# Kernel tuning notes

Measured on AMD Instinct MI355X. Metric: run time of the kernel, lower is better.

## Reference

```python
import jax, jax.numpy as jnp
import numpy as np

B, C, H, W = 32, 256, 64, 64
MH = 8
E = 524288
TEMPERATURE = 0.1
LN_EPS = 1e-5


def setup_inputs() -> dict:
    key = jax.random.key(0)
    ks = jax.random.split(key, 6)
    n_nodes = B * H * W
    scale = 1.0 / np.sqrt(C).astype(np.float32)
    img = jax.random.normal(ks[0], (B, C, H, W), jnp.float32)
    all_edge = jax.random.randint(ks[1], (2, E), 0, n_nodes, dtype=jnp.int64)
    Wp = jax.random.normal(ks[2], (C, C), jnp.float32) * scale
    bp = jnp.zeros((C,), jnp.float32)
    Wg = jax.random.normal(ks[3], (C, C), jnp.float32) * scale
    bg = jnp.zeros((C,), jnp.float32)
    ln_gamma = jnp.ones((C,), jnp.float32)
    ln_beta = jnp.zeros((C,), jnp.float32)
    diff_query = jax.random.normal(ks[4], (1, 1, C), jnp.float32) * scale  # xavier-ish
    return {"img": img, "all_edge": all_edge, "Wp": Wp, "bp": bp,
            "Wg": Wg, "bg": bg, "ln_gamma": ln_gamma, "ln_beta": ln_beta,
            "diff_query": diff_query, "mask_head": MH}


def _gcn_conv(x, row, col, Wg, bg, num_nodes):
    # PyG GCNConv with add_self_loops=True, symmetric normalization.
    loop = jnp.arange(num_nodes, dtype=row.dtype)
    row = jnp.concatenate([row, loop])
    col = jnp.concatenate([col, loop])
    deg = jnp.zeros((num_nodes,), x.dtype).at[col].add(1.0)
    dinv = jnp.where(deg > 0, jax.lax.rsqrt(deg), 0.0)
    norm = dinv[row] * dinv[col]                      # [E+N]
    xl = x @ Wg                                       # [N, C]
    msg = xl[row] * norm[:, None]                     # gather + scale
    agg = jax.ops.segment_sum(msg, col, num_segments=num_nodes)
    return agg + bg


def reference(img, all_edge, Wp, bp, Wg, bg, ln_gamma, ln_beta, diff_query, mask_head):
    b, c, h, w = img.shape
    node_num = h * w
    num_nodes = b * node_num
    hd = c // mask_head
    # [B,C,H,W] -> [B, N, C]
    x = jnp.transpose(img, (0, 2, 3, 1)).reshape(b, node_num, c)
    x = x @ Wp + bp
    x = x.reshape(num_nodes, c)
    g = _gcn_conv(x, all_edge[0], all_edge[1], Wg, bg, num_nodes)
    g = jax.nn.gelu(g, approximate=False)             # nn.GELU (exact)
    g = g + x
    mu = jnp.mean(g, axis=-1, keepdims=True)
    var = jnp.mean(jnp.square(g - mu), axis=-1, keepdims=True)
    img_graph = (g - mu) * jax.lax.rsqrt(var + LN_EPS) * ln_gamma + ln_beta
    # multi-head adjacency: query [B*MH, 1, hd], keys [B*MH, N, hd]
    q = jnp.broadcast_to(diff_query, (b, 1, c)).reshape(b * mask_head, 1, hd)
    k = img_graph.reshape(b, node_num, mask_head, hd)
    k = jnp.transpose(k, (0, 2, 1, 3)).reshape(b * mask_head, node_num, hd)
    adj = jnp.einsum('bod,bnd->bon', q, k) / TEMPERATURE
    adj = jax.nn.softmax(adj, axis=-1)
    return img_graph, adj
```

## Files before the change

kernel.cpp:

```cpp
#include <hip/hip_runtime.h>
#include <hip/hip_bf16.h>

typedef unsigned short u16;
typedef __attribute__((ext_vector_type(8))) short short8;
typedef __attribute__((ext_vector_type(16))) float f32x16;

#define AS1C(p) ((const __attribute__((address_space(1))) void*)(p))
#define AS3(p)  ((__attribute__((address_space(3))) void*)(p))

constexpr int CC    = 256;
constexpr int HWSZ  = 4096;
constexpr int NNODE = 131072;
constexpr int EEDG  = 524288;
constexpr int CAP   = 32;

__device__ __forceinline__ float bf2f(u16 h){ unsigned u = ((unsigned)h)<<16; float f; __builtin_memcpy(&f,&u,4); return f; }
__device__ __forceinline__ u16 f2bf(float f){ unsigned u; __builtin_memcpy(&u,&f,4); return (u16)((u + 0x7FFFu + ((u>>16)&1u))>>16); }

__device__ __forceinline__ unsigned pkbf(float a, float b){
  float2 t; t.x = a; t.y = b;
  __hip_bfloat162 h = __float22bfloat162_rn(t);
  unsigned u; __builtin_memcpy(&u,&h,4); return u;
}

__device__ __forceinline__ float gelu_fast(float v){
  float y = 0.7978845608f*(v + 0.044715f*v*v*v);
  float e = __expf(2.0f*y);
  float r = __builtin_amdgcn_rcpf(e + 1.0f);
  return 0.5f*v*(2.0f - 2.0f*r);
}

__device__ __forceinline__ void unpack8(uint4 q, float f[8]){
  unsigned w0=q.x,w1=q.y,w2=q.z,w3=q.w;
  unsigned l0=w0<<16, h0=w0&0xffff0000u, l1=w1<<16, h1=w1&0xffff0000u;
  unsigned l2=w2<<16, h2=w2&0xffff0000u, l3=w3<<16, h3=w3&0xffff0000u;
  __builtin_memcpy(&f[0],&l0,4); __builtin_memcpy(&f[1],&h0,4);
  __builtin_memcpy(&f[2],&l1,4); __builtin_memcpy(&f[3],&h1,4);
  __builtin_memcpy(&f[4],&l2,4); __builtin_memcpy(&f[5],&h2,4);
  __builtin_memcpy(&f[6],&l3,4); __builtin_memcpy(&f[7],&h3,4);
}

__global__ __launch_bounds__(256) void transpose_split(const float* __restrict__ src,
                                                       u16* __restrict__ dhi, u16* __restrict__ dlo,
                                                       int R, int Ccols, size_t sb_in, size_t sb_out)
{
  __shared__ float t[64][65];
  const float* s = src + blockIdx.z*sb_in + (size_t)(blockIdx.y*64)*Ccols + blockIdx.x*64;
  size_t obase   = blockIdx.z*sb_out + (size_t)(blockIdx.x*64)*R + blockIdx.y*64;
  int tid = threadIdx.x;
  for (int i=0;i<4;++i){
    int idx = i*256 + tid;
    int r = idx>>4, q = idx&15;
    float4 v = *(const float4*)(s + (size_t)r*Ccols + q*4);
    t[r][q*4+0]=v.x; t[r][q*4+1]=v.y; t[r][q*4+2]=v.z; t[r][q*4+3]=v.w;
  }
  __syncthreads();
  for (int i=0;i<2;++i){
    int idx = i*256 + tid;
    int rr = idx>>3, ch = idx&7;
    u16 hi[8], lo[8];
    for (int j=0;j<8;++j){
      float f = t[ch*8+j][rr];
      u16 h = f2bf(f); hi[j] = h;
      lo[j] = f2bf(f - bf2f(h));
    }
    *(uint4*)(dhi + obase + (size_t)rr*R + ch*8) = *(uint4*)hi;
    if (dlo) *(uint4*)(dlo + obase + (size_t)rr*R + ch*8) = *(uint4*)lo;
  }
}

__global__ __launch_bounds__(256,3) void gemm_t1(const float* __restrict__ img,
                                                 const u16* __restrict__ Bt,
                                                 const float* __restrict__ bias,
                                                 u16* __restrict__ C)
{
  __shared__ u16 As[2][64*32];
  __shared__ u16 Bs[2][256*32];
  const int tid = threadIdx.x, wid = tid>>6, lane = tid&63;
  const int row0 = blockIdx.x*64;
  const int bb = row0>>12, hw0 = row0&4095;
  const float* abase = img + (size_t)bb*CC*HWSZ + hw0;
  const int l31 = lane&31, lh = lane>>5;
  const int mpr = l31;
  const int cb  = wid*8 + lh*4;
  const int cs  = wid ^ (mpr&3);
  const int wa0 = (2*mpr  )*32 + cs*8 + lh*4;
  const int wa1 = (2*mpr+1)*32 + cs*8 + lh*4;

  f32x16 acc[2][2];
  #pragma unroll
  for (int i=0;i<2;++i)
    #pragma unroll
    for (int j=0;j<2;++j)
      #pragma unroll
      for (int e=0;e<16;++e) acc[i][j][e]=0.f;

  float2 arX[4], arY[4];

#define LOADA(dst, kt)                                                                 \
  { _Pragma("unroll")                                                                  \
    for (int i=0;i<4;++i)                                                              \
      dst[i] = *(const float2*)(abase + (size_t)((kt)+cb+i)*HWSZ + 2*mpr); }

#define WRITEA(buf, src)                                                               \
  { uint2 p0, p1;                                                                      \
    p0.x = pkbf(src[0].x, src[1].x); p0.y = pkbf(src[2].x, src[3].x);                  \
    p1.x = pkbf(src[0].y, src[1].y); p1.y = pkbf(src[2].y, src[3].y);                  \
    *(uint2*)&As[buf][wa0] = p0;                                                       \
    *(uint2*)&As[buf][wa1] = p1; }

#define STAGE_B(buf, kt)                                                               \
  { _Pragma("unroll")                                                                  \
    for (int it=0; it<4; ++it){                                                        \
      int qb = (it*4+wid)*64;                                                          \
      int q  = qb + lane;                                                              \
      int m  = q>>2, sc = q&3;                                                         \
      int gs = sc ^ ((m>>1)&3);                                                        \
      __builtin_amdgcn_global_load_lds(AS1C(Bt + (size_t)m*256 + (kt) + gs*8),         \
                                       AS3(&Bs[buf][qb*8]), 16, 0, 0); } }

#define STEP(t, XR, YR)                                                                \
  { const int cur = (t)&1;                                                             \
    if ((t) < 7) STAGE_B(cur^1, ((t)+1)*32)                                            \
    if ((t) < 6) LOADA(YR, ((t)+2)*32)                                                 \
    short8 af[2][2], bfr[2][2];                                                        \
    _Pragma("unroll")                                                                  \
    for (int fm=0; fm<2; ++fm)                                                         \
      _Pragma("unroll")                                                                \
      for (int kh=0; kh<2; ++kh) {                                                     \
        int row = fm*32 + l31;                                                         \
        int sa  = (kh*2 + lh) ^ ((row>>1)&3);                                          \
        af[fm][kh] = *(const short8*)&As[cur][row*32 + sa*8];                          \
      }                                                                                \
    _Pragma("unroll")                                                                  \
    for (int fn=0; fn<2; ++fn)                                                         \
      _Pragma("unroll")                                                                \
      for (int kh=0; kh<2; ++kh) {                                                     \
        int col = wid*64 + fn*32 + l31;                                                \
        int sb  = (kh*2 + lh) ^ ((col>>1)&3);                                          \
        bfr[fn][kh] = *(const short8*)&Bs[cur][col*32 + sb*8];                         \
      }                                                                                \
    _Pragma("unroll")                                                                  \
    for (int kh=0; kh<2; ++kh)                                                         \
      _Pragma("unroll")                                                                \
      for (int fm=0; fm<2; ++fm)                                                       \
        _Pragma("unroll")                                                              \
        for (int fn=0; fn<2; ++fn)                                                     \
          acc[fm][fn] = __builtin_amdgcn_mfma_f32_32x32x16_bf16(af[fm][kh], bfr[fn][kh], acc[fm][fn], 0, 0, 0); \
    if ((t) < 7) {                                                                     \
      WRITEA(cur^1, XR)                                                                \
      if ((t) < 6) { asm volatile("s_waitcnt vmcnt(8) lgkmcnt(0)" ::: "memory"); }     \
      else         { asm volatile("s_waitcnt vmcnt(0) lgkmcnt(0)" ::: "memory"); }     \
      __builtin_amdgcn_s_barrier();                                                    \
      __builtin_amdgcn_sched_barrier(0);                                               \
    } }

  LOADA(arX, 0)
  STAGE_B(0, 0)
  asm volatile("s_waitcnt vmcnt(4)" ::: "memory");
  WRITEA(0, arX)
  LOADA(arX, 32)
  asm volatile("s_waitcnt vmcnt(8) lgkmcnt(0)" ::: "memory");
  __builtin_amdgcn_s_barrier();
  __builtin_amdgcn_sched_barrier(0);

  for (int tt=0; tt<8; tt+=2) {
    STEP(tt,   arX, arY)
    STEP(tt+1, arY, arX)
  }
#undef STEP
#undef STAGE_B
#undef WRITEA
#undef LOADA

  #pragma unroll
  for (int fn=0; fn<2; ++fn) {
    int col = wid*64 + fn*32 + l31;
    float bv = bias ? bias[col] : 0.f;
    #pragma unroll
    for (int fm=0; fm<2; ++fm) {
      int rbase = row0 + fm*32 + 4*lh;
      #pragma unroll
      for (int reg=0; reg<16; ++reg) {
        int row = rbase + (reg&3) + 8*(reg>>2);
        C[(size_t)row*256 + col] = f2bf(acc[fm][fn][reg] + bv);
      }
    }
  }
}

__global__ __launch_bounds__(256,3) void gemm1p(const u16* __restrict__ A,
                                                const u16* __restrict__ Bt,
                                                const float* __restrict__ bias,
                                                u16* __restrict__ C)
{
  __shared__ u16 As[2][64*32];
  __shared__ u16 Bs[2][256*32];
  const int tid = threadIdx.x, wid = tid>>6, lane = tid&63;
  const int row0 = blockIdx.x*64;
  const int l31 = lane&31, lh = lane>>5;

  f32x16 acc[2][2];
  #pragma unroll
  for (int i=0;i<2;++i)
    #pragma unroll
    for (int j=0;j<2;++j)
      #pragma unroll
      for (int e=0;e<16;++e) acc[i][j][e]=0.f;

#define STAGE_AB(buf, kt)                                                              \
  {                                                                                    \
    {                                                                                  \
      int qb = wid*64;                                                                 \
      int q  = qb + lane;                                                              \
      int m  = q>>2, sc = q&3;                                                         \
      int gs = sc ^ ((m>>1)&3);                                                        \
      __builtin_amdgcn_global_load_lds(AS1C(A + (size_t)(row0+m)*256 + (kt) + gs*8),   \
                                       AS3(&As[buf][qb*8]), 16, 0, 0);                 \
    }                                                                                  \
    _Pragma("unroll")                                                                  \
    for (int it=0; it<4; ++it){                                                        \
      int qb = (it*4+wid)*64;                                                          \
      int q  = qb + lane;                                                              \
      int m  = q>>2, sc = q&3;                                                         \
      int gs = sc ^ ((m>>1)&3);                                                        \
      __builtin_amdgcn_global_load_lds(AS1C(Bt + (size_t)m*256 + (kt) + gs*8),         \
                                       AS3(&Bs[buf][qb*8]), 16, 0, 0);                 \
    }                                                                                  \
  }

  STAGE_AB(0, 0)
  asm volatile("s_waitcnt vmcnt(0)" ::: "memory");
  __syncthreads();

  for (int t=0; t<8; ++t) {
    int cur = t&1;
    if (t<7) STAGE_AB(cur^1, (t+1)*32)

    short8 af[2][2], bfr[2][2];
    #pragma unroll
    for (int fm=0; fm<2; ++fm)
      #pragma unroll
      for (int kh=0; kh<2; ++kh) {
        int row = fm*32 + l31;
        int sa  = (kh*2 + lh) ^ ((row>>1)&3);
        af[fm][kh] = *(const short8*)&As[cur][row*32 + sa*8];
      }
    #pragma unroll
    for (int fn=0; fn<2; ++fn)
      #pragma unroll
      for (int kh=0; kh<2; ++kh) {
        int col = wid*64 + fn*32 + l31;
        int sb  = (kh*2 + lh) ^ ((col>>1)&3);
        bfr[fn][kh] = *(const short8*)&Bs[cur][col*32 + sb*8];
      }
    #pragma unroll
    for (int kh=0; kh<2; ++kh)
      #pragma unroll
      for (int fm=0; fm<2; ++fm)
        #pragma unroll
        for (int fn=0; fn<2; ++fn)
          acc[fm][fn] = __builtin_amdgcn_mfma_f32_32x32x16_bf16(af[fm][kh], bfr[fn][kh], acc[fm][fn], 0, 0, 0);
    asm volatile("s_waitcnt vmcnt(0)" ::: "memory");
    __syncthreads();
  }
#undef STAGE_AB

  #pragma unroll
  for (int fn=0; fn<2; ++fn) {
    int col = wid*64 + fn*32 + l31;
    float bv = bias ? bias[col] : 0.f;
    #pragma unroll
    for (int fm=0; fm<2; ++fm) {
      int rbase = row0 + fm*32 + 4*lh;
      #pragma unroll
      for (int reg=0; reg<16; ++reg) {
        int row = rbase + (reg&3) + 8*(reg>>2);
        C[(size_t)row*256 + col] = f2bf(acc[fm][fn][reg] + bv);
      }
    }
  }
}

__global__ void fill_all(const int* __restrict__ row, const int* __restrict__ col,
                         int* __restrict__ cur, int* __restrict__ bucket){
  int e = blockIdx.x*256 + threadIdx.x;
  if (e >= EEDG) return;
  int c = col[e];
  int s = atomicAdd(&cur[c], 1);
  if (s < CAP) bucket[(size_t)c*CAP + s] = row[e];
}
__global__ void calc_dinv(const int* __restrict__ cnt, float* __restrict__ dinv){
  int n = blockIdx.x*256 + threadIdx.x;
  if (n < NNODE) dinv[n] = rsqrtf((float)cnt[n] + 1.0f);
}

__global__ __launch_bounds__(256) void fused_agg(
    const u16* __restrict__ xl, const u16* __restrict__ xhi,
    const int* __restrict__ cnt, const float* __restrict__ dinv, const int* __restrict__ bucket,
    const float* __restrict__ bgv, const float* __restrict__ gam, const float* __restrict__ bet,
    const float* __restrict__ qv, float* __restrict__ outg, float* __restrict__ logits)
{
  const int wid = threadIdx.x>>6, lane = threadIdx.x&63;
  const int half = lane>>5, sl = lane&31;
  const int n = blockIdx.x*8 + wid*2 + half;
  const int c0 = sl*8;
  const float dn = dinv[n];
  int lim = cnt[n]; if (lim > CAP) lim = CAP;

  int rl = bucket[(size_t)n*CAP + sl];
  if (sl >= lim) rl = n;
  float wl = (sl < lim) ? dinv[rl]*dn : 0.0f;

  uint4 qh = *(const uint4*)(xhi + (size_t)n*256 + c0);

  float a[8];
  {
    uint4 q = *(const uint4*)(xl + (size_t)n*256 + c0);
    unpack8(q, a);
    float wself = dn*dn;
    #pragma unroll
    for (int j=0;j<8;++j) a[j] *= wself;
  }

  int limR = (lim + 3) & ~3;
  for (int s=0; s<limR; s+=4) {
    int b0 = half*32 + s;
    int  r0 = __shfl(rl, b0),   r1 = __shfl(rl, b0+1);
    int  r2 = __shfl(rl, b0+2), r3 = __shfl(rl, b0+3);
    float w0 = __shfl(wl, b0),   w1 = __shfl(wl, b0+1);
    float w2 = __shfl(wl, b0+2), w3 = __shfl(wl, b0+3);
    uint4 q0 = *(const uint4*)(xl + (size_t)r0*256 + c0);
    uint4 q1 = *(const uint4*)(xl + (size_t)r1*256 + c0);
    uint4 q2 = *(const uint4*)(xl + (size_t)r2*256 + c0);
    uint4 q3 = *(const uint4*)(xl + (size_t)r3*256 + c0);
    float f0[8], f1[8], f2[8], f3[8];
    unpack8(q0, f0); unpack8(q1, f1); unpack8(q2, f2); unpack8(q3, f3);
    #pragma unroll
    for (int j=0;j<8;++j) a[j] += f0[j]*w0 + f1[j]*w1 + f2[j]*w2 + f3[j]*w3;
  }

  float xv[8];
  unpack8(qh, xv);

  float4 b0v = *(const float4*)(bgv + c0), b1v = *(const float4*)(bgv + c0 + 4);
  float bgs[8] = {b0v.x,b0v.y,b0v.z,b0v.w,b1v.x,b1v.y,b1v.z,b1v.w};
  float g[8];
  float s1 = 0.f, s2 = 0.f;
  #pragma unroll
  for (int j=0;j<8;++j){
    g[j] = gelu_fast(a[j] + bgs[j]) + xv[j];
    s1 += g[j]; s2 += g[j]*g[j];
  }
  #pragma unroll
  for (int off=16; off; off>>=1){ s1 += __shfl_xor(s1, off); s2 += __shfl_xor(s2, off); }
  float mu  = s1*(1.0f/256.0f);
  float var = s2*(1.0f/256.0f) - mu*mu;
  float inv = rsqrtf(var + 1e-5f);

  float4 g0 = *(const float4*)(gam + c0), g1 = *(const float4*)(gam + c0 + 4);
  float4 e0 = *(const float4*)(bet + c0), e1 = *(const float4*)(bet + c0 + 4);
  float gms[8] = {g0.x,g0.y,g0.z,g0.w,g1.x,g1.y,g1.z,g1.w};
  float bts[8] = {e0.x,e0.y,e0.z,e0.w,e1.x,e1.y,e1.z,e1.w};
  float y[8];
  #pragma unroll
  for (int j=0;j<8;++j) y[j] = (g[j]-mu)*inv*gms[j] + bts[j];

  float4 o0 = {y[0],y[1],y[2],y[3]}, o1 = {y[4],y[5],y[6],y[7]};
  *reinterpret_cast<float4*>(outg + (size_t)n*256 + c0)     = o0;
  *reinterpret_cast<float4*>(outg + (size_t)n*256 + c0 + 4) = o1;

  float4 q0 = *(const float4*)(qv + c0), q1 = *(const float4*)(qv + c0 + 4);
  float qs[8] = {q0.x,q0.y,q0.z,q0.w,q1.x,q1.y,q1.z,q1.w};
  float dq = 0.f;
  #pragma unroll
  for (int j=0;j<8;++j) dq += y[j]*qs[j];
  dq += __shfl_xor(dq,1); dq += __shfl_xor(dq,2);
  if ((sl&3)==0){
    int b = n>>12, p = n&4095, h = sl>>2;
    logits[(size_t)(b*8+h)*4096 + p] = dq*10.0f;
  }
}

__global__ __launch_bounds__(256) void softmax_rows(const float* __restrict__ logits, float* __restrict__ outa){
  int r = blockIdx.x;
  const float* p = logits + (size_t)r*4096;
  int tid = threadIdx.x;
  int wid = tid>>6, lane = tid&63;
  __shared__ float redm[4];
  __shared__ float reds[4];
  float v[16];
  float mx = -1e30f;
  for (int i=0;i<16;++i){ v[i] = p[tid + i*256]; mx = fmaxf(mx, v[i]); }
  for (int off=32; off; off>>=1) mx = fmaxf(mx, __shfl_xor(mx, off));
  if (lane==0) redm[wid]=mx;
  __syncthreads();
  mx = fmaxf(fmaxf(redm[0],redm[1]), fmaxf(redm[2],redm[3]));
  float sum = 0.f;
  for (int i=0;i<16;++i){ v[i] = expf(v[i]-mx); sum += v[i]; }
  for (int off=32; off; off>>=1) sum += __shfl_xor(sum, off);
  if (lane==0) reds[wid]=sum;
  __syncthreads();
  sum = reds[0]+reds[1]+reds[2]+reds[3];
  float rinv = 1.0f/sum;
  for (int i=0;i<16;++i) outa[(size_t)r*4096 + tid + i*256] = v[i]*rinv;
}

extern "C" void kernel_launch(void* const* d_in, const int* in_sizes, int n_in,
                              void* d_out, int out_size, void* d_ws, size_t ws_size,
                              hipStream_t stream)
{
  const float* img  = (const float*)d_in[0];
  const int* edges  = (const int*)d_in[1];
  const float* Wp   = (const float*)d_in[2];
  const float* bp   = (const float*)d_in[3];
  const float* Wg   = (const float*)d_in[4];
  const float* bg   = (const float*)d_in[5];
  const float* lng  = (const float*)d_in[6];
  const float* lnb  = (const float*)d_in[7];
  const float* dq   = (const float*)d_in[8];
  char* ws = (char*)d_ws;

  constexpr size_t REG  = (size_t)NNODE*CC*2;
  constexpr size_t WTS  = 2u*131072;
  constexpr size_t GBLK = 524288u*2 + (size_t)NNODE*CAP*4 + (size_t)256*4096*4;
  if (ws_size < 2*REG + WTS + GBLK) return;

  u16* buf0 = (u16*)(ws + 0);
  u16* buf1 = (u16*)(ws + REG);
  char* wts  = ws + 2*REG;
  char* gblk = wts + WTS;

  u16* WpT_hi = (u16*)(wts);
  u16* WgT_hi = (u16*)(wts + 131072);
  int*   cur    = (int*)(gblk);
  float* dinv   = (float*)(gblk + 524288);
  int*   bucket = (int*)(gblk + 1048576);
  float* logits = (float*)(gblk + 1048576 + (size_t)NNODE*CAP*4);

  transpose_split<<<dim3(4,4,1), 256, 0, stream>>>(Wp, WpT_hi, nullptr, 256, 256, 0, 0);
  transpose_split<<<dim3(4,4,1), 256, 0, stream>>>(Wg, WgT_hi, nullptr, 256, 256, 0, 0);

  hipMemsetAsync(cur, 0, 524288, stream);
  fill_all <<<2048, 256, 0, stream>>>(edges, edges+EEDG, cur, bucket);
  calc_dinv<<<512,  256, 0, stream>>>(cur, dinv);

  gemm_t1<<<2048, 256, 0, stream>>>(img, WpT_hi, bp, buf0);
  gemm1p<<<2048, 256, 0, stream>>>(buf0, WgT_hi, nullptr, buf1);

  float* outg = (float*)d_out;
  float* outa = (float*)d_out + (size_t)NNODE*CC;
  fused_agg<<<NNODE/8, 256, 0, stream>>>(buf1, buf0, cur, dinv, bucket,
                                         bg, lng, lnb, dq, outg, logits);
  softmax_rows<<<256, 256, 0, stream>>>(logits, outa);
}
```

Baseline: 230.1 us.

## Fold Wp·Wg into combined weight and compute x and xl in one dual GEMM

Precomputes W2 = Wp·Wg and the folded bias bp·Wg, then uses a single GEMM kernel that reads img once and produces both x (via Wp) and xl (via W2) with two accumulator sets. This removes the second pass over the 64 MB bf16 intermediate x and one kernel launch. In exchange each block uses twice the B-tile LDS and accumulators, and occupancy drops from 3 to 2 blocks per SM. Numerics also change slightly because xl no longer comes from bf16-rounded x.

```diff
diff --git a/kernel.cpp b/kernel.cpp
--- a/kernel.cpp
+++ b/kernel.cpp
@@ -69,13 +69,35 @@
   }
 }
 
-__global__ __launch_bounds__(256,3) void gemm_t1(const float* __restrict__ img,
-                                                 const u16* __restrict__ Bt,
-                                                 const float* __restrict__ bias,
-                                                 u16* __restrict__ C)
+__global__ __launch_bounds__(256) void split_rm(const float* __restrict__ src, u16* __restrict__ dhi)
+{
+  int i = blockIdx.x*256 + threadIdx.x;
+  float4 v = ((const float4*)src)[i];
+  ushort4 h;
+  h.x = f2bf(v.x); h.y = f2bf(v.y); h.z = f2bf(v.z); h.w = f2bf(v.w);
+  ((ushort4*)dhi)[i] = h;
+}
+
+__global__ void bias2_k(const float* __restrict__ bp, const float* __restrict__ Wg,
+                        float* __restrict__ b2)
+{
+  int n = threadIdx.x;
+  float s = 0.f;
+  for (int k=0;k<256;++k) s += bp[k]*Wg[(size_t)k*256 + n];
+  b2[n] = s;
+}
+
+__global__ __launch_bounds__(256,2) void gemm_dual(const float* __restrict__ img,
+                                                   const u16* __restrict__ Btp,
+                                                   const u16* __restrict__ Bt2,
+                                                   const float* __restrict__ bias1,
+                                                   const float* __restrict__ bias2,
+                                                   u16* __restrict__ Cx,
+                                                   u16* __restrict__ Cxl)
 {
   __shared__ u16 As[2][64*32];
-  __shared__ u16 Bs[2][256*32];
+  __shared__ u16 Bsp[2][256*32];
+  __shared__ u16 Bs2[2][256*32];
   const int tid = threadIdx.x, wid = tid>>6, lane = tid&63;
   const int row0 = blockIdx.x*64;
   const int bb = row0>>12, hw0 = row0&4095;
@@ -87,13 +109,13 @@
   const int wa0 = (2*mpr  )*32 + cs*8 + lh*4;
   const int wa1 = (2*mpr+1)*32 + cs*8 + lh*4;
 
-  f32x16 acc[2][2];
+  f32x16 accx[2][2], accl[2][2];
   #pragma unroll
   for (int i=0;i<2;++i)
     #pragma unroll
     for (int j=0;j<2;++j)
       #pragma unroll
-      for (int e=0;e<16;++e) acc[i][j][e]=0.f;
+      for (int e=0;e<16;++e){ accx[i][j][e]=0.f; accl[i][j][e]=0.f; }
 
   float2 arX[4], arY[4];
 
@@ -116,14 +138,16 @@
       int q  = qb + lane;                                                              \
       int m  = q>>2, sc = q&3;                                                         \
       int gs = sc ^ ((m>>1)&3);                                                        \
-      __builtin_amdgcn_global_load_lds(AS1C(Bt + (size_t)m*256 + (kt) + gs*8),         \
-                                       AS3(&Bs[buf][qb*8]), 16, 0, 0); } }
+      __builtin_amdgcn_global_load_lds(AS1C(Btp + (size_t)m*256 + (kt) + gs*8),        \
+                                       AS3(&Bsp[buf][qb*8]), 16, 0, 0);                \
+      __builtin_amdgcn_global_load_lds(AS1C(Bt2 + (size_t)m*256 + (kt) + gs*8),        \
+                                       AS3(&Bs2[buf][qb*8]), 16, 0, 0); } }
 
 #define STEP(t, XR, YR)                                                                \
   { const int cur = (t)&1;                                                             \
     if ((t) < 7) STAGE_B(cur^1, ((t)+1)*32)                                            \
     if ((t) < 6) LOADA(YR, ((t)+2)*32)                                                 \
-    short8 af[2][2], bfr[2][2];                                                        \
+    short8 af[2][2], bp8[2][2], b28[2][2];                                             \
     _Pragma("unroll")                                                                  \
     for (int fm=0; fm<2; ++fm)                                                         \
       _Pragma("unroll")                                                                \
@@ -138,18 +162,21 @@
       for (int kh=0; kh<2; ++kh) {                                                     \
         int col = wid*64 + fn*32 + l31;                                                \
         int sb  = (kh*2 + lh) ^ ((col>>1)&3);                                          \
-        bfr[fn][kh] = *(const short8*)&Bs[cur][col*32 + sb*8];                         \
+        bp8[fn][kh] = *(const short8*)&Bsp[cur][col*32 + sb*8];                        \
+        b28[fn][kh] = *(const short8*)&Bs2[cur][col*32 + sb*8];                        \
       }                                                                                \
     _Pragma("unroll")                                                                  \
     for (int kh=0; kh<2; ++kh)                                                         \
       _Pragma("unroll")                                                                \
       for (int fm=0; fm<2; ++fm)                                                       \
         _Pragma("unroll")                                                              \
-        for (int fn=0; fn<2; ++fn)                                                     \
-          acc[fm][fn] = __builtin_amdgcn_mfma_f32_32x32x16_bf16(af[fm][kh], bfr[fn][kh], acc[fm][fn], 0, 0, 0); \
+        for (int fn=0; fn<2; ++fn) {                                                   \
+          accx[fm][fn] = __builtin_amdgcn_mfma_f32_32x32x16_bf16(af[fm][kh], bp8[fn][kh], accx[fm][fn], 0, 0, 0); \
+          accl[fm][fn] = __builtin_amdgcn_mfma_f32_32x32x16_bf16(af[fm][kh], b28[fn][kh], accl[fm][fn], 0, 0, 0); \
+        }                                                                              \
     if ((t) < 7) {                                                                     \
       WRITEA(cur^1, XR)                                                                \
-      if ((t) < 6) { asm volatile("s_waitcnt vmcnt(8) lgkmcnt(0)" ::: "memory"); }     \
+      if ((t) < 6) { asm volatile("s_waitcnt vmcnt(4) lgkmcnt(0)" ::: "memory"); }     \
       else         { asm volatile("s_waitcnt vmcnt(0) lgkmcnt(0)" ::: "memory"); }     \
       __builtin_amdgcn_s_barrier();                                                    \
       __builtin_amdgcn_sched_barrier(0);                                               \
@@ -157,10 +184,10 @@
 
   LOADA(arX, 0)
   STAGE_B(0, 0)
-  asm volatile("s_waitcnt vmcnt(4)" ::: "memory");
+  asm volatile("s_waitcnt vmcnt(8)" ::: "memory");
   WRITEA(0, arX)
   LOADA(arX, 32)
-  asm volatile("s_waitcnt vmcnt(8) lgkmcnt(0)" ::: "memory");
+  asm volatile("s_waitcnt vmcnt(4) lgkmcnt(0)" ::: "memory");
   __builtin_amdgcn_s_barrier();
   __builtin_amdgcn_sched_barrier(0);
 
@@ -176,14 +203,16 @@
   #pragma unroll
   for (int fn=0; fn<2; ++fn) {
     int col = wid*64 + fn*32 + l31;
-    float bv = bias ? bias[col] : 0.f;
+    float b1 = bias1 ? bias1[col] : 0.f;
+    float b2 = bias2 ? bias2[col] : 0.f;
     #pragma unroll
     for (int fm=0; fm<2; ++fm) {
       int rbase = row0 + fm*32 + 4*lh;
       #pragma unroll
       for (int reg=0; reg<16; ++reg) {
         int row = rbase + (reg&3) + 8*(reg>>2);
-        C[(size_t)row*256 + col] = f2bf(acc[fm][fn][reg] + bv);
+        Cx [(size_t)row*256 + col] = f2bf(accx[fm][fn][reg] + b1);
+        Cxl[(size_t)row*256 + col] = f2bf(accl[fm][fn][reg] + b2);
       }
     }
   }
@@ -422,7 +451,7 @@
   char* ws = (char*)d_ws;
 
   constexpr size_t REG  = (size_t)NNODE*CC*2;
-  constexpr size_t WTS  = 2u*131072;
+  constexpr size_t WTS  = 4u*131072 + 4096;
   constexpr size_t GBLK = 524288u*2 + (size_t)NNODE*CAP*4 + (size_t)256*4096*4;
   if (ws_size < 2*REG + WTS + GBLK) return;
 
@@ -433,6 +462,9 @@
 
   u16* WpT_hi = (u16*)(wts);
   u16* WgT_hi = (u16*)(wts + 131072);
+  u16* Wp_rm  = (u16*)(wts + 262144);
+  u16* W2T_hi = (u16*)(wts + 393216);
+  float* bias2 = (float*)(wts + 524288);
   int*   cur    = (int*)(gblk);
   float* dinv   = (float*)(gblk + 524288);
   int*   bucket = (int*)(gblk + 1048576);
@@ -440,13 +472,15 @@
 
   transpose_split<<<dim3(4,4,1), 256, 0, stream>>>(Wp, WpT_hi, nullptr, 256, 256, 0, 0);
   transpose_split<<<dim3(4,4,1), 256, 0, stream>>>(Wg, WgT_hi, nullptr, 256, 256, 0, 0);
+  split_rm<<<64, 256, 0, stream>>>(Wp, Wp_rm);
+  gemm1p<<<4, 256, 0, stream>>>(WgT_hi, Wp_rm, nullptr, W2T_hi);
+  bias2_k<<<1, 256, 0, stream>>>(bp, Wg, bias2);
 
   hipMemsetAsync(cur, 0, 524288, stream);
   fill_all <<<2048, 256, 0, stream>>>(edges, edges+EEDG, cur, bucket);
   calc_dinv<<<512,  256, 0, stream>>>(cur, dinv);
 
-  gemm_t1<<<2048, 256, 0, stream>>>(img, WpT_hi, bp, buf0);
-  gemm1p<<<2048, 256, 0, stream>>>(buf0, WgT_hi, nullptr, buf1);
+  gemm_dual<<<2048, 256, 0, stream>>>(img, WpT_hi, W2T_hi, bp, bias2, buf0, buf1);
 
   float* outg = (float*)d_out;
   float* outa = (float*)d_out + (size_t)NNODE*CC;
```

After: 250.0 us. 8.7% more time.
